# Kernel tuning notes

Hardware: AMD Instinct MI355X
Metric: run time of the kernel (lower is better)

Reference implementation:

```python
import jax, jax.numpy as jnp
import numpy as np

BN_EPS = 1e-5
LRELU_SLOPE = 0.2
EPS = 1e-8
K = 3


def setup_inputs() -> dict:
    key = jax.random.key(0)
    ks = jax.random.split(key, 8)
    B, Cd, Cs, M, S, N = 8, 256, 512, 4096, 1024, 4096
    return {
        "dense_data": jax.random.normal(ks[0], (B, Cd, M), dtype=jnp.float32),
        "dense_idx": jax.random.randint(ks[1], (B, M), 0, N),
        "sparse_data": jax.random.normal(ks[2], (B, Cs, S), dtype=jnp.float32),
        "sparse_idx": jax.random.randint(ks[3], (B, S), 0, N),
        "pcd": jax.random.normal(ks[4], (B, 3, N), dtype=jnp.float32),
        "conv_w": jax.random.normal(ks[5], (Cd, 3 * Cd), dtype=jnp.float32) * (1.0 / np.sqrt(3 * Cd)),
        "bn_gamma": jnp.ones((Cd,), dtype=jnp.float32),
        "bn_beta": jnp.zeros((Cd,), dtype=jnp.float32),
    }


def _knn_interpolate(dense_xyz, sparse_xyz, sparse_feats, k):
    # dense_xyz: [B,3,M], sparse_xyz: [B,3,S], sparse_feats: [B,Cs,S]
    d2 = (
        jnp.sum(dense_xyz**2, axis=1)[:, :, None]
        + jnp.sum(sparse_xyz**2, axis=1)[:, None, :]
        - 2.0 * jnp.einsum("bdm,bds->bms", dense_xyz, sparse_xyz)
    )  # [B,M,S] squared distances
    neg_d, idx = jax.lax.top_k(-d2, k)  # [B,M,K]
    d_nb = -neg_d
    w = 1.0 / (d_nb + EPS)
    w = w / jnp.sum(w, axis=-1, keepdims=True)  # [B,M,K]
    # gather neighbor features: [B,Cs,M,K]
    nb = jnp.take_along_axis(sparse_feats[:, :, None, :], idx[:, None, :, :], axis=3)
    return jnp.sum(nb * w[:, None, :, :], axis=-1)  # [B,Cs,M]


def reference(dense_data, dense_idx, sparse_data, sparse_idx, pcd, conv_w, bn_gamma, bn_beta):
    # gather xyz coords of dense / sparse points: [B,3,M], [B,3,S]
    dense_xyz = jnp.take_along_axis(pcd, dense_idx[:, None, :], axis=2)
    sparse_xyz = jnp.take_along_axis(pcd, sparse_idx[:, None, :], axis=2)
    interp = _knn_interpolate(dense_xyz, sparse_xyz, sparse_data, K)  # [B,Cs,M]
    x = jnp.concatenate([dense_data, interp], axis=1)  # [B,3*Cd,M]
    # 1x1 conv (no bias)
    y = jnp.einsum("oc,bcm->bom", conv_w, x)
    # BatchNorm1d (training mode: batch statistics over B and M, biased var)
    mu = jnp.mean(y, axis=(0, 2), keepdims=True)
    var = jnp.mean((y - mu) ** 2, axis=(0, 2), keepdims=True)
    y = (y - mu) * jax.lax.rsqrt(var + BN_EPS)
    y = y * bn_gamma[None, :, None] + bn_beta[None, :, None]
    # LeakyReLU(0.2)
    y = jnp.where(y >= 0, y, LRELU_SLOPE * y)
    return (y, dense_idx)
```

## Files before the change

kernel.cpp:

```cpp
#include <hip/hip_runtime.h>
#include <float.h>

#define DEVI __device__ __forceinline__

namespace {

constexpr int NB   = 8;
constexpr int CD   = 256;
constexpr int CS   = 512;
constexpr int MM   = 4096;
constexpr int SS   = 1024;
constexpr int NN   = 4096;
constexpr int KTOT = 768;
constexpr int OC   = 256;
constexpr float KEPS  = 1e-8f;
constexpr float BNEPS = 1e-5f;
constexpr float SLOPE = 0.2f;

constexpr size_t OFF_Z    = 0;
constexpr size_t SZ_Z     = (size_t)NB * SS * OC * 4;
constexpr size_t OFF_IDX3 = OFF_Z + SZ_Z;
constexpr size_t SZ_IDX3  = (size_t)NB * MM * 3 * 4;
constexpr size_t OFF_W3   = OFF_IDX3 + SZ_IDX3;
constexpr size_t OFF_WBF  = OFF_W3 + SZ_IDX3;
constexpr size_t SZ_WBF   = (size_t)OC * KTOT * 2;
constexpr size_t OFF_PS   = OFF_WBF + SZ_WBF;
constexpr size_t SZ_PS    = (size_t)512 * OC * 4;
constexpr size_t OFF_PS2  = OFF_PS + SZ_PS;
constexpr size_t OFF_A    = OFF_PS2 + SZ_PS;
constexpr size_t OFF_B    = OFF_A + 1024;

typedef __attribute__((ext_vector_type(8))) short s16x8;
typedef __attribute__((ext_vector_type(4))) float f32x4;

DEVI short f2bf(float f) {
  union { float f; unsigned u; } c; c.f = f;
  unsigned r = c.u + 0x7fffu + ((c.u >> 16) & 1u);
  return (short)(r >> 16);
}

__global__ __launch_bounds__(256) void k_knn(
    const int* __restrict__ didx, const int* __restrict__ sidx,
    const float* __restrict__ pcd,
    int* __restrict__ idx3, float* __restrict__ w3,
    float* __restrict__ outIdxF,
    const float* __restrict__ convw, short* __restrict__ wbf) {
  __shared__ float4 sxyz[SS];
  __shared__ float  pd[4][64][3];
  __shared__ int    pi[4][64][3];

  int blk = blockIdx.x;
  int b   = blk >> 6;
  int m0  = (blk & 63) << 6;
  int tid = threadIdx.x;
  const float* pb = pcd + (size_t)b * 3 * NN;

  for (int i = tid; i < 384; i += 256) {
    int g = blk * 384 + i;
    wbf[g] = f2bf(convw[g]);
  }

  for (int s = tid; s < SS; s += 256) {
    int si = sidx[b * SS + s];
    sxyz[s] = make_float4(pb[si], pb[NN + si], pb[2 * NN + si], 0.f);
  }

  int p     = tid & 63;
  int chunk = tid >> 6;
  int m     = m0 + p;
  int di    = didx[b * MM + m];
  float px = pb[di], py = pb[NN + di], pz = pb[2 * NN + di];

  if (chunk == 0) outIdxF[b * MM + m] = (float)di;

  __syncthreads();

  float d0 = FLT_MAX, d1 = FLT_MAX, d2 = FLT_MAX;
  int   i0 = 0, i1 = 0, i2 = 0;
  int s0c = chunk << 8;
#pragma unroll 4
  for (int t = 0; t < 256; ++t) {
    int s = s0c + t;
    float4 c = sxyz[s];
    float dx = c.x - px, dy = c.y - py, dz = c.z - pz;
    float d  = dx * dx + dy * dy + dz * dz;
    bool lt0 = d < d0, lt1 = d < d1, lt2 = d < d2;
    d2 = lt1 ? d1 : (lt2 ? d : d2);  i2 = lt1 ? i1 : (lt2 ? s : i2);
    d1 = lt0 ? d0 : (lt1 ? d : d1);  i1 = lt0 ? i0 : (lt1 ? s : i1);
    d0 = lt0 ? d  : d0;              i0 = lt0 ? s : i0;
  }
  pd[chunk][p][0] = d0; pd[chunk][p][1] = d1; pd[chunk][p][2] = d2;
  pi[chunk][p][0] = i0; pi[chunk][p][1] = i1; pi[chunk][p][2] = i2;
  __syncthreads();

  if (tid < 64) {
    float e0 = FLT_MAX, e1 = FLT_MAX, e2 = FLT_MAX;
    int   j0 = 0, j1 = 0, j2 = 0;
#pragma unroll
    for (int c = 0; c < 4; ++c)
#pragma unroll
      for (int r = 0; r < 3; ++r) {
        float d = pd[c][p][r]; int s = pi[c][p][r];
        bool lt0 = d < e0, lt1 = d < e1, lt2 = d < e2;
        e2 = lt1 ? e1 : (lt2 ? d : e2);  j2 = lt1 ? j1 : (lt2 ? s : j2);
        e1 = lt0 ? e0 : (lt1 ? d : e1);  j1 = lt0 ? j0 : (lt1 ? s : j1);
        e0 = lt0 ? d  : e0;              j0 = lt0 ? s : j0;
      }
    float w0 = 1.f / (e0 + KEPS), w1 = 1.f / (e1 + KEPS), w2 = 1.f / (e2 + KEPS);
    float inv = 1.f / (w0 + w1 + w2);
    int base = (b * MM + m) * 3;
    idx3[base] = j0; idx3[base + 1] = j1; idx3[base + 2] = j2;
    w3[base] = w0 * inv; w3[base + 1] = w1 * inv; w3[base + 2] = w2 * inv;
  }
}

__global__ __launch_bounds__(256) void k_gemmZ(
    const float* __restrict__ sp, const short* __restrict__ wbf,
    float* __restrict__ Z) {
  __shared__ __align__(16) short Wl[256 * 72];
  __shared__ __align__(16) short Sl[32 * 72];

  int blk = blockIdx.x;
  int st = blk & 31, b = blk >> 5;
  int s0 = st * 32;
  int tid = threadIdx.x, wv = tid >> 6, lane = tid & 63;
  int lo = lane & 15, quad = lane >> 4;

  f32x4 acc[4][2] = {};
  for (int k0 = 0; k0 < CS; k0 += 64) {
    __syncthreads();
#pragma unroll
    for (int r = 0; r < 8; ++r) {
      int lin = r * 256 + tid, row = lin >> 3, c8 = lin & 7;
      uint4 v = *(const uint4*)((const unsigned short*)wbf + (size_t)row * KTOT + CD + k0 + c8 * 8);
      *(uint4*)(&Wl[row * 72 + c8 * 8]) = v;
    }
#pragma unroll
    for (int r = 0; r < 2; ++r) {
      int lin = r * 256 + tid, cc = lin >> 3, s4 = lin & 7;
      float4 v = *(const float4*)(sp + (size_t)(b * CS + k0 + cc) * SS + s0 + s4 * 4);
      Sl[(s4 * 4 + 0) * 72 + cc] = f2bf(v.x);
      Sl[(s4 * 4 + 1) * 72 + cc] = f2bf(v.y);
      Sl[(s4 * 4 + 2) * 72 + cc] = f2bf(v.z);
      Sl[(s4 * 4 + 3) * 72 + cc] = f2bf(v.w);
    }
    __syncthreads();
    s16x8 af[2][4], bfr[2][2];
#pragma unroll
    for (int h = 0; h < 2; ++h) {
#pragma unroll
      for (int i = 0; i < 4; ++i)
        af[h][i] = *(const s16x8*)(&Wl[(wv * 64 + i * 16 + lo) * 72 + h * 32 + quad * 8]);
#pragma unroll
      for (int j = 0; j < 2; ++j)
        bfr[h][j] = *(const s16x8*)(&Sl[(j * 16 + lo) * 72 + h * 32 + quad * 8]);
    }
#pragma unroll
    for (int h = 0; h < 2; ++h)
#pragma unroll
      for (int i = 0; i < 4; ++i)
#pragma unroll
        for (int j = 0; j < 2; ++j)
          acc[i][j] = __builtin_amdgcn_mfma_f32_16x16x32_bf16(af[h][i], bfr[h][j], acc[i][j], 0, 0, 0);
  }
#pragma unroll
  for (int i = 0; i < 4; ++i)
#pragma unroll
    for (int j = 0; j < 2; ++j) {
      int s = j * 16 + lo, o = wv * 64 + i * 16 + quad * 4;
      *(f32x4*)(Z + (size_t)(b * SS + s0 + s) * OC + o) = acc[i][j];
    }
}

__global__ __launch_bounds__(256) void k_gemmDC(
    const float* __restrict__ dense, const float* __restrict__ Z,
    const int* __restrict__ idx3, const float* __restrict__ w3,
    const short* __restrict__ wbf, float* __restrict__ y,
    float* __restrict__ ps, float* __restrict__ ps2) {
  __shared__ __align__(16) short Wl[256 * 72];
  __shared__ __align__(16) short Xl[64 * 72];
  __shared__ int   mi3[192];
  __shared__ float mw3[192];

  int blk = blockIdx.x;
  int mt = blk & 63, b = blk >> 6, m0 = mt << 6;
  int tid = threadIdx.x, wv = tid >> 6, lane = tid & 63;
  int lo = lane & 15, quad = lane >> 4;

  {
    int base = (b * MM + m0) * 3;
    for (int i = tid; i < 192; i += 256) { mi3[i] = idx3[base + i]; mw3[i] = w3[base + i]; }
  }

  f32x4 acc[4][4] = {};
  for (int k0 = 0; k0 < CD; k0 += 64) {
    __syncthreads();
#pragma unroll
    for (int r = 0; r < 8; ++r) {
      int lin = r * 256 + tid, row = lin >> 3, c8 = lin & 7;
      uint4 v = *(const uint4*)((const unsigned short*)wbf + (size_t)row * KTOT + k0 + c8 * 8);
      *(uint4*)(&Wl[row * 72 + c8 * 8]) = v;
    }
    {
      int kk4 = tid >> 4, m4 = tid & 15;
      float4 v0 = *(const float4*)(dense + (size_t)(b * CD + k0 + kk4 * 4 + 0) * MM + m0 + m4 * 4);
      float4 v1 = *(const float4*)(dense + (size_t)(b * CD + k0 + kk4 * 4 + 1) * MM + m0 + m4 * 4);
      float4 v2 = *(const float4*)(dense + (size_t)(b * CD + k0 + kk4 * 4 + 2) * MM + m0 + m4 * 4);
      float4 v3 = *(const float4*)(dense + (size_t)(b * CD + k0 + kk4 * 4 + 3) * MM + m0 + m4 * 4);
      ushort4 w;
      w.x = (unsigned short)f2bf(v0.x); w.y = (unsigned short)f2bf(v1.x);
      w.z = (unsigned short)f2bf(v2.x); w.w = (unsigned short)f2bf(v3.x);
      *(ushort4*)(&Xl[(m4 * 4 + 0) * 72 + kk4 * 4]) = w;
      w.x = (unsigned short)f2bf(v0.y); w.y = (unsigned short)f2bf(v1.y);
      w.z = (unsigned short)f2bf(v2.y); w.w = (unsigned short)f2bf(v3.y);
      *(ushort4*)(&Xl[(m4 * 4 + 1) * 72 + kk4 * 4]) = w;
      w.x = (unsigned short)f2bf(v0.z); w.y = (unsigned short)f2bf(v1.z);
      w.z = (unsigned short)f2bf(v2.z); w.w = (unsigned short)f2bf(v3.z);
      *(ushort4*)(&Xl[(m4 * 4 + 2) * 72 + kk4 * 4]) = w;
      w.x = (unsigned short)f2bf(v0.w); w.y = (unsigned short)f2bf(v1.w);
      w.z = (unsigned short)f2bf(v2.w); w.w = (unsigned short)f2bf(v3.w);
      *(ushort4*)(&Xl[(m4 * 4 + 3) * 72 + kk4 * 4]) = w;
    }
    __syncthreads();
    s16x8 af[2][4], bfr[2][4];
#pragma unroll
    for (int h = 0; h < 2; ++h) {
#pragma unroll
      for (int i = 0; i < 4; ++i)
        af[h][i] = *(const s16x8*)(&Wl[(wv * 64 + i * 16 + lo) * 72 + h * 32 + quad * 8]);
#pragma unroll
      for (int j = 0; j < 4; ++j)
        bfr[h][j] = *(const s16x8*)(&Xl[(j * 16 + lo) * 72 + h * 32 + quad * 8]);
    }
#pragma unroll
    for (int h = 0; h < 2; ++h)
#pragma unroll
      for (int i = 0; i < 4; ++i)
#pragma unroll
        for (int j = 0; j < 4; ++j)
          acc[i][j] = __builtin_amdgcn_mfma_f32_16x16x32_bf16(af[h][i], bfr[h][j], acc[i][j], 0, 0, 0);
  }

  float* P = (float*)Wl;
  const float* Zb = Z + (size_t)b * SS * OC;
  float ss[4][4] = {}, s2s[4][4] = {};
  __syncthreads();

#pragma unroll
  for (int h = 0; h < 2; ++h) {
#pragma unroll 4
    for (int ml = 0; ml < 32; ++ml) {
      int mg = (h * 32 + ml) * 3;
      float p = mw3[mg + 0] * Zb[(size_t)mi3[mg + 0] * OC + tid]
              + mw3[mg + 1] * Zb[(size_t)mi3[mg + 1] * OC + tid]
              + mw3[mg + 2] * Zb[(size_t)mi3[mg + 2] * OC + tid];
      P[ml * 260 + tid] = p;
    }
    __syncthreads();
#pragma unroll
    for (int i = 0; i < 4; ++i)
#pragma unroll
      for (int jj = 0; jj < 2; ++jj) {
        int j = h * 2 + jj, ml = jj * 16 + lo;
        int o = wv * 64 + i * 16 + quad * 4;
        f32x4 p = *(const f32x4*)(&P[ml * 260 + o]);
        f32x4 v = acc[i][j] + p;
        float* dst = y + (size_t)(b * OC + o) * MM + m0 + j * 16 + lo;
#pragma unroll
        for (int r = 0; r < 4; ++r) {
          float vv = v[r];
          dst[(size_t)r * MM] = vv;
          ss[i][r] += vv; s2s[i][r] += vv * vv;
        }
      }
    __syncthreads();
  }

#pragma unroll
  for (int i = 0; i < 4; ++i)
#pragma unroll
    for (int r = 0; r < 4; ++r) {
      float a = ss[i][r], q = s2s[i][r];
      for (int off = 1; off < 16; off <<= 1) { a += __shfl_xor(a, off); q += __shfl_xor(q, off); }
      ss[i][r] = a; s2s[i][r] = q;
    }
  if (lo == 0) {
#pragma unroll
    for (int i = 0; i < 4; ++i)
#pragma unroll
      for (int r = 0; r < 4; ++r) {
        int o = wv * 64 + i * 16 + quad * 4 + r;
        ps[(size_t)blk * OC + o]  = ss[i][r];
        ps2[(size_t)blk * OC + o] = s2s[i][r];
      }
  }
}

__global__ void k_finalize(const float* __restrict__ ps, const float* __restrict__ ps2,
                           const float* __restrict__ gamma, const float* __restrict__ beta,
                           float* __restrict__ sA, float* __restrict__ sB) {
  int o = threadIdx.x;
  float s = 0.f, s2 = 0.f;
#pragma unroll 8
  for (int k = 0; k < 512; ++k) { s += ps[k * OC + o]; s2 += ps2[k * OC + o]; }
  float mn = s / (float)(NB * MM);
  float vr = s2 / (float)(NB * MM) - mn * mn;
  float a  = rsqrtf(vr + BNEPS) * gamma[o];
  sA[o] = a;
  sB[o] = beta[o] - mn * a;
}

__global__ void k_norm(float* __restrict__ y, const float* __restrict__ sA,
                       const float* __restrict__ sB) {
  int i = blockIdx.x * 256 + threadIdx.x;
  int o = (i >> 10) & 255;
  float a = sA[o], be = sB[o];
  float4 v = ((const float4*)y)[i];
  float t;
  t = v.x * a + be; v.x = t >= 0.f ? t : SLOPE * t;
  t = v.y * a + be; v.y = t >= 0.f ? t : SLOPE * t;
  t = v.z * a + be; v.z = t >= 0.f ? t : SLOPE * t;
  t = v.w * a + be; v.w = t >= 0.f ? t : SLOPE * t;
  ((float4*)y)[i] = v;
}

}

extern "C" void kernel_launch(void* const* d_in, const int* in_sizes, int n_in,
                              void* d_out, int out_size, void* d_ws, size_t ws_size,
                              hipStream_t stream) {
  const float* dense = (const float*)d_in[0];
  const int*   didx  = (const int*)d_in[1];
  const float* sp    = (const float*)d_in[2];
  const int*   sidx  = (const int*)d_in[3];
  const float* pcd   = (const float*)d_in[4];
  const float* convw = (const float*)d_in[5];
  const float* gamma = (const float*)d_in[6];
  const float* beta  = (const float*)d_in[7];

  float* y = (float*)d_out;
  float* outIdxF = y + (size_t)NB * OC * MM;

  char* ws = (char*)d_ws;
  float* Z    = (float*)(ws + OFF_Z);
  int*   idx3 = (int*)(ws + OFF_IDX3);
  float* w3   = (float*)(ws + OFF_W3);
  short* wbf  = (short*)(ws + OFF_WBF);
  float* ps   = (float*)(ws + OFF_PS);
  float* ps2  = (float*)(ws + OFF_PS2);
  float* sA   = (float*)(ws + OFF_A);
  float* sB   = (float*)(ws + OFF_B);

  k_knn     <<<NB * (MM / 64), 256, 0, stream>>>(didx, sidx, pcd, idx3, w3, outIdxF, convw, wbf);
  k_gemmZ   <<<NB * (SS / 32), 256, 0, stream>>>(sp, wbf, Z);
  k_gemmDC  <<<NB * (MM / 64), 256, 0, stream>>>(dense, Z, idx3, w3, wbf, y, ps, ps2);
  k_finalize<<<1, 256, 0, stream>>>(ps, ps2, gamma, beta, sA, sB);
  k_norm    <<<(NB * OC * MM / 4) / 256, 256, 0, stream>>>(y, sA, sB);
}
```

Before: 193.5 us.

## Merge kNN and sparse GEMM into one launch; convert weights inline; direct Z gather

```diff
diff --git a/kernel.cpp b/kernel.cpp
--- a/kernel.cpp
+++ b/kernel.cpp
@@ -22,9 +22,7 @@
 constexpr size_t OFF_IDX3 = OFF_Z + SZ_Z;
 constexpr size_t SZ_IDX3  = (size_t)NB * MM * 3 * 4;
 constexpr size_t OFF_W3   = OFF_IDX3 + SZ_IDX3;
-constexpr size_t OFF_WBF  = OFF_W3 + SZ_IDX3;
-constexpr size_t SZ_WBF   = (size_t)OC * KTOT * 2;
-constexpr size_t OFF_PS   = OFF_WBF + SZ_WBF;
+constexpr size_t OFF_PS   = OFF_W3 + SZ_IDX3;
 constexpr size_t SZ_PS    = (size_t)512 * OC * 4;
 constexpr size_t OFF_PS2  = OFF_PS + SZ_PS;
 constexpr size_t OFF_A    = OFF_PS2 + SZ_PS;
@@ -39,143 +37,146 @@
   return (short)(r >> 16);
 }
 
-__global__ __launch_bounds__(256) void k_knn(
+__global__ __launch_bounds__(256) void k_pre(
     const int* __restrict__ didx, const int* __restrict__ sidx,
-    const float* __restrict__ pcd,
+    const float* __restrict__ pcd, const float* __restrict__ sp,
+    const float* __restrict__ convw,
     int* __restrict__ idx3, float* __restrict__ w3,
-    float* __restrict__ outIdxF,
-    const float* __restrict__ convw, short* __restrict__ wbf) {
-  __shared__ float4 sxyz[SS];
-  __shared__ float  pd[4][64][3];
-  __shared__ int    pi[4][64][3];
-
-  int blk = blockIdx.x;
-  int b   = blk >> 6;
-  int m0  = (blk & 63) << 6;
+    float* __restrict__ outIdxF, float* __restrict__ Z) {
+  __shared__ __align__(16) char smem[41472];
+
   int tid = threadIdx.x;
-  const float* pb = pcd + (size_t)b * 3 * NN;
-
-  for (int i = tid; i < 384; i += 256) {
-    int g = blk * 384 + i;
-    wbf[g] = f2bf(convw[g]);
-  }
-
-  for (int s = tid; s < SS; s += 256) {
-    int si = sidx[b * SS + s];
-    sxyz[s] = make_float4(pb[si], pb[NN + si], pb[2 * NN + si], 0.f);
-  }
-
-  int p     = tid & 63;
-  int chunk = tid >> 6;
-  int m     = m0 + p;
-  int di    = didx[b * MM + m];
-  float px = pb[di], py = pb[NN + di], pz = pb[2 * NN + di];
-
-  if (chunk == 0) outIdxF[b * MM + m] = (float)di;
-
-  __syncthreads();
-
-  float d0 = FLT_MAX, d1 = FLT_MAX, d2 = FLT_MAX;
-  int   i0 = 0, i1 = 0, i2 = 0;
-  int s0c = chunk << 8;
+
+  if (blockIdx.x < 512) {
+    float4* sxyz = (float4*)smem;
+    float*  pd   = (float*)(smem + 16384);
+    int*    pi   = (int*)(smem + 16384 + 3072);
+
+    int blk = blockIdx.x;
+    int b   = blk >> 6;
+    int m0  = (blk & 63) << 6;
+    const float* pb = pcd + (size_t)b * 3 * NN;
+
+    for (int s = tid; s < SS; s += 256) {
+      int si = sidx[b * SS + s];
+      sxyz[s] = make_float4(pb[si], pb[NN + si], pb[2 * NN + si], 0.f);
+    }
+
+    int p     = tid & 63;
+    int chunk = tid >> 6;
+    int m     = m0 + p;
+    int di    = didx[b * MM + m];
+    float px = pb[di], py = pb[NN + di], pz = pb[2 * NN + di];
+
+    if (chunk == 0) outIdxF[b * MM + m] = (float)di;
+
+    __syncthreads();
+
+    float d0 = FLT_MAX, d1 = FLT_MAX, d2 = FLT_MAX;
+    int   i0 = 0, i1 = 0, i2 = 0;
+    int s0c = chunk << 8;
 #pragma unroll 4
-  for (int t = 0; t < 256; ++t) {
-    int s = s0c + t;
-    float4 c = sxyz[s];
-    float dx = c.x - px, dy = c.y - py, dz = c.z - pz;
-    float d  = dx * dx + dy * dy + dz * dz;
-    bool lt0 = d < d0, lt1 = d < d1, lt2 = d < d2;
-    d2 = lt1 ? d1 : (lt2 ? d : d2);  i2 = lt1 ? i1 : (lt2 ? s : i2);
-    d1 = lt0 ? d0 : (lt1 ? d : d1);  i1 = lt0 ? i0 : (lt1 ? s : i1);
-    d0 = lt0 ? d  : d0;              i0 = lt0 ? s : i0;
-  }
-  pd[chunk][p][0] = d0; pd[chunk][p][1] = d1; pd[chunk][p][2] = d2;
-  pi[chunk][p][0] = i0; pi[chunk][p][1] = i1; pi[chunk][p][2] = i2;
-  __syncthreads();
-
-  if (tid < 64) {
-    float e0 = FLT_MAX, e1 = FLT_MAX, e2 = FLT_MAX;
-    int   j0 = 0, j1 = 0, j2 = 0;
-#pragma unroll
-    for (int c = 0; c < 4; ++c)
-#pragma unroll
-      for (int r = 0; r < 3; ++r) {
-        float d = pd[c][p][r]; int s = pi[c][p][r];
-        bool lt0 = d < e0, lt1 = d < e1, lt2 = d < e2;
-        e2 = lt1 ? e1 : (lt2 ? d : e2);  j2 = lt1 ? j1 : (lt2 ? s : j2);
-        e1 = lt0 ? e0 : (lt1 ? d : e1);  j1 = lt0 ? j0 : (lt1 ? s : j1);
-        e0 = lt0 ? d  : e0;              j0 = lt0 ? s : j0;
-      }
-    float w0 = 1.f / (e0 + KEPS), w1 = 1.f / (e1 + KEPS), w2 = 1.f / (e2 + KEPS);
-    float inv = 1.f / (w0 + w1 + w2);
-    int base = (b * MM + m) * 3;
-    idx3[base] = j0; idx3[base + 1] = j1; idx3[base + 2] = j2;
-    w3[base] = w0 * inv; w3[base + 1] = w1 * inv; w3[base + 2] = w2 * inv;
-  }
-}
-
-__global__ __launch_bounds__(256) void k_gemmZ(
-    const float* __restrict__ sp, const short* __restrict__ wbf,
-    float* __restrict__ Z) {
-  __shared__ __align__(16) short Wl[256 * 72];
-  __shared__ __align__(16) short Sl[32 * 72];
-
-  int blk = blockIdx.x;
-  int st = blk & 31, b = blk >> 5;
-  int s0 = st * 32;
-  int tid = threadIdx.x, wv = tid >> 6, lane = tid & 63;
-  int lo = lane & 15, quad = lane >> 4;
-
-  f32x4 acc[4][2] = {};
-  for (int k0 = 0; k0 < CS; k0 += 64) {
+    for (int t = 0; t < 256; ++t) {
+      int s = s0c + t;
+      float4 c = sxyz[s];
+      float dx = c.x - px, dy = c.y - py, dz = c.z - pz;
+      float d  = dx * dx + dy * dy + dz * dz;
+      bool lt0 = d < d0, lt1 = d < d1, lt2 = d < d2;
+      d2 = lt1 ? d1 : (lt2 ? d : d2);  i2 = lt1 ? i1 : (lt2 ? s : i2);
+      d1 = lt0 ? d0 : (lt1 ? d : d1);  i1 = lt0 ? i0 : (lt1 ? s : i1);
+      d0 = lt0 ? d  : d0;              i0 = lt0 ? s : i0;
+    }
+    pd[(chunk * 64 + p) * 3 + 0] = d0; pd[(chunk * 64 + p) * 3 + 1] = d1; pd[(chunk * 64 + p) * 3 + 2] = d2;
+    pi[(chunk * 64 + p) * 3 + 0] = i0; pi[(chunk * 64 + p) * 3 + 1] = i1; pi[(chunk * 64 + p) * 3 + 2] = i2;
     __syncthreads();
-#pragma unroll
-    for (int r = 0; r < 8; ++r) {
-      int lin = r * 256 + tid, row = lin >> 3, c8 = lin & 7;
-      uint4 v = *(const uint4*)((const unsigned short*)wbf + (size_t)row * KTOT + CD + k0 + c8 * 8);
-      *(uint4*)(&Wl[row * 72 + c8 * 8]) = v;
-    }
-#pragma unroll
-    for (int r = 0; r < 2; ++r) {
-      int lin = r * 256 + tid, cc = lin >> 3, s4 = lin & 7;
-      float4 v = *(const float4*)(sp + (size_t)(b * CS + k0 + cc) * SS + s0 + s4 * 4);
-      Sl[(s4 * 4 + 0) * 72 + cc] = f2bf(v.x);
-      Sl[(s4 * 4 + 1) * 72 + cc] = f2bf(v.y);
-      Sl[(s4 * 4 + 2) * 72 + cc] = f2bf(v.z);
-      Sl[(s4 * 4 + 3) * 72 + cc] = f2bf(v.w);
-    }
-    __syncthreads();
-    s16x8 af[2][4], bfr[2][2];
-#pragma unroll
-    for (int h = 0; h < 2; ++h) {
-#pragma unroll
-      for (int i = 0; i < 4; ++i)
-        af[h][i] = *(const s16x8*)(&Wl[(wv * 64 + i * 16 + lo) * 72 + h * 32 + quad * 8]);
-#pragma unroll
-      for (int j = 0; j < 2; ++j)
-        bfr[h][j] = *(const s16x8*)(&Sl[(j * 16 + lo) * 72 + h * 32 + quad * 8]);
-    }
-#pragma unroll
-    for (int h = 0; h < 2; ++h)
-#pragma unroll
-      for (int i = 0; i < 4; ++i)
+
+    if (tid < 64) {
+      float e0 = FLT_MAX, e1 = FLT_MAX, e2 = FLT_MAX;
+      int   j0 = 0, j1 = 0, j2 = 0;
+#pragma unroll
+      for (int c = 0; c < 4; ++c)
+#pragma unroll
+        for (int r = 0; r < 3; ++r) {
+          float d = pd[(c * 64 + p) * 3 + r]; int s = pi[(c * 64 + p) * 3 + r];
+          bool lt0 = d < e0, lt1 = d < e1, lt2 = d < e2;
+          e2 = lt1 ? e1 : (lt2 ? d : e2);  j2 = lt1 ? j1 : (lt2 ? s : j2);
+          e1 = lt0 ? e0 : (lt1 ? d : e1);  j1 = lt0 ? j0 : (lt1 ? s : j1);
+          e0 = lt0 ? d  : e0;              j0 = lt0 ? s : j0;
+        }
+      float w0 = 1.f / (e0 + KEPS), w1 = 1.f / (e1 + KEPS), w2 = 1.f / (e2 + KEPS);
+      float inv = 1.f / (w0 + w1 + w2);
+      int base = (b * MM + m) * 3;
+      idx3[base] = j0; idx3[base + 1] = j1; idx3[base + 2] = j2;
+      w3[base] = w0 * inv; w3[base + 1] = w1 * inv; w3[base + 2] = w2 * inv;
+    }
+  } else {
+    short* Wl = (short*)smem;
+    short* Sl = (short*)(smem + 256 * 72 * 2);
+
+    int blk = blockIdx.x - 512;
+    int st = blk & 31, b = blk >> 5;
+    int s0 = st * 32;
+    int wv = tid >> 6, lane = tid & 63;
+    int lo = lane & 15, quad = lane >> 4;
+
+    f32x4 acc[4][2] = {};
+    for (int k0 = 0; k0 < CS; k0 += 64) {
+      __syncthreads();
+#pragma unroll
+      for (int r = 0; r < 8; ++r) {
+        int lin = r * 256 + tid, row = lin >> 3, c8 = lin & 7;
+        const float* src = convw + (size_t)row * KTOT + CD + k0 + c8 * 8;
+        float4 va = *(const float4*)src, vb = *(const float4*)(src + 4);
+        ushort4 plo, phi;
+        plo.x = (unsigned short)f2bf(va.x); plo.y = (unsigned short)f2bf(va.y);
+        plo.z = (unsigned short)f2bf(va.z); plo.w = (unsigned short)f2bf(va.w);
+        phi.x = (unsigned short)f2bf(vb.x); phi.y = (unsigned short)f2bf(vb.y);
+        phi.z = (unsigned short)f2bf(vb.z); phi.w = (unsigned short)f2bf(vb.w);
+        *(ushort4*)(&Wl[row * 72 + c8 * 8])     = plo;
+        *(ushort4*)(&Wl[row * 72 + c8 * 8 + 4]) = phi;
+      }
+#pragma unroll
+      for (int r = 0; r < 2; ++r) {
+        int lin = r * 256 + tid, cc = lin >> 3, s4 = lin & 7;
+        float4 v = *(const float4*)(sp + (size_t)(b * CS + k0 + cc) * SS + s0 + s4 * 4);
+        Sl[(s4 * 4 + 0) * 72 + cc] = f2bf(v.x);
+        Sl[(s4 * 4 + 1) * 72 + cc] = f2bf(v.y);
+        Sl[(s4 * 4 + 2) * 72 + cc] = f2bf(v.z);
+        Sl[(s4 * 4 + 3) * 72 + cc] = f2bf(v.w);
+      }
+      __syncthreads();
+      s16x8 af[2][4], bfr[2][2];
+#pragma unroll
+      for (int h = 0; h < 2; ++h) {
+#pragma unroll
+        for (int i = 0; i < 4; ++i)
+          af[h][i] = *(const s16x8*)(&Wl[(wv * 64 + i * 16 + lo) * 72 + h * 32 + quad * 8]);
 #pragma unroll
         for (int j = 0; j < 2; ++j)
-          acc[i][j] = __builtin_amdgcn_mfma_f32_16x16x32_bf16(af[h][i], bfr[h][j], acc[i][j], 0, 0, 0);
-  }
-#pragma unroll
-  for (int i = 0; i < 4; ++i)
-#pragma unroll
-    for (int j = 0; j < 2; ++j) {
-      int s = j * 16 + lo, o = wv * 64 + i * 16 + quad * 4;
-      *(f32x4*)(Z + (size_t)(b * SS + s0 + s) * OC + o) = acc[i][j];
-    }
+          bfr[h][j] = *(const s16x8*)(&Sl[(j * 16 + lo) * 72 + h * 32 + quad * 8]);
+      }
+#pragma unroll
+      for (int h = 0; h < 2; ++h)
+#pragma unroll
+        for (int i = 0; i < 4; ++i)
+#pragma unroll
+          for (int j = 0; j < 2; ++j)
+            acc[i][j] = __builtin_amdgcn_mfma_f32_16x16x32_bf16(af[h][i], bfr[h][j], acc[i][j], 0, 0, 0);
+    }
+#pragma unroll
+    for (int i = 0; i < 4; ++i)
+#pragma unroll
+      for (int j = 0; j < 2; ++j) {
+        int s = j * 16 + lo, o = wv * 64 + i * 16 + quad * 4;
+        *(f32x4*)(Z + (size_t)(b * SS + s0 + s) * OC + o) = acc[i][j];
+      }
+  }
 }
 
 __global__ __launch_bounds__(256) void k_gemmDC(
     const float* __restrict__ dense, const float* __restrict__ Z,
     const int* __restrict__ idx3, const float* __restrict__ w3,
-    const short* __restrict__ wbf, float* __restrict__ y,
+    const float* __restrict__ convw, float* __restrict__ y,
     float* __restrict__ ps, float* __restrict__ ps2) {
   __shared__ __align__(16) short Wl[256 * 72];
   __shared__ __align__(16) short Xl[64 * 72];
@@ -198,8 +199,15 @@
 #pragma unroll
     for (int r = 0; r < 8; ++r) {
       int lin = r * 256 + tid, row = lin >> 3, c8 = lin & 7;
-      uint4 v = *(const uint4*)((const unsigned short*)wbf + (size_t)row * KTOT + k0 + c8 * 8);
-      *(uint4*)(&Wl[row * 72 + c8 * 8]) = v;
+      const float* src = convw + (size_t)row * KTOT + k0 + c8 * 8;
+      float4 va = *(const float4*)src, vb = *(const float4*)(src + 4);
+      ushort4 plo, phi;
+      plo.x = (unsigned short)f2bf(va.x); plo.y = (unsigned short)f2bf(va.y);
+      plo.z = (unsigned short)f2bf(va.z); plo.w = (unsigned short)f2bf(va.w);
+      phi.x = (unsigned short)f2bf(vb.x); phi.y = (unsigned short)f2bf(vb.y);
+      phi.z = (unsigned short)f2bf(vb.z); phi.w = (unsigned short)f2bf(vb.w);
+      *(ushort4*)(&Wl[row * 72 + c8 * 8])     = plo;
+      *(ushort4*)(&Wl[row * 72 + c8 * 8 + 4]) = phi;
     }
     {
       int kk4 = tid >> 4, m4 = tid & 15;
@@ -241,39 +249,31 @@
           acc[i][j] = __builtin_amdgcn_mfma_f32_16x16x32_bf16(af[h][i], bfr[h][j], acc[i][j], 0, 0, 0);
   }
 
-  float* P = (float*)Wl;
   const float* Zb = Z + (size_t)b * SS * OC;
   float ss[4][4] = {}, s2s[4][4] = {};
-  __syncthreads();
-
-#pragma unroll
-  for (int h = 0; h < 2; ++h) {
-#pragma unroll 4
-    for (int ml = 0; ml < 32; ++ml) {
-      int mg = (h * 32 + ml) * 3;
-      float p = mw3[mg + 0] * Zb[(size_t)mi3[mg + 0] * OC + tid]
-              + mw3[mg + 1] * Zb[(size_t)mi3[mg + 1] * OC + tid]
-              + mw3[mg + 2] * Zb[(size_t)mi3[mg + 2] * OC + tid];
-      P[ml * 260 + tid] = p;
-    }
-    __syncthreads();
-#pragma unroll
-    for (int i = 0; i < 4; ++i)
-#pragma unroll
-      for (int jj = 0; jj < 2; ++jj) {
-        int j = h * 2 + jj, ml = jj * 16 + lo;
-        int o = wv * 64 + i * 16 + quad * 4;
-        f32x4 p = *(const f32x4*)(&P[ml * 260 + o]);
-        f32x4 v = acc[i][j] + p;
-        float* dst = y + (size_t)(b * OC + o) * MM + m0 + j * 16 + lo;
-#pragma unroll
-        for (int r = 0; r < 4; ++r) {
-          float vv = v[r];
-          dst[(size_t)r * MM] = vv;
-          ss[i][r] += vv; s2s[i][r] += vv * vv;
-        }
-      }
-    __syncthreads();
+#pragma unroll
+  for (int j = 0; j < 4; ++j) {
+    int ml = j * 16 + lo;
+    int r0 = mi3[ml * 3 + 0], r1 = mi3[ml * 3 + 1], r2 = mi3[ml * 3 + 2];
+    float w0 = mw3[ml * 3 + 0], w1 = mw3[ml * 3 + 1], w2 = mw3[ml * 3 + 2];
+    const float* z0 = Zb + (size_t)r0 * OC;
+    const float* z1 = Zb + (size_t)r1 * OC;
+    const float* z2 = Zb + (size_t)r2 * OC;
+#pragma unroll
+    for (int i = 0; i < 4; ++i) {
+      int o = wv * 64 + i * 16 + quad * 4;
+      f32x4 p = w0 * *(const f32x4*)(z0 + o)
+              + w1 * *(const f32x4*)(z1 + o)
+              + w2 * *(const f32x4*)(z2 + o);
+      f32x4 v = acc[i][j] + p;
+      float* dst = y + (size_t)(b * OC + o) * MM + m0 + ml;
+#pragma unroll
+      for (int r = 0; r < 4; ++r) {
+        float vv = v[r];
+        dst[(size_t)r * MM] = vv;
+        ss[i][r] += vv; s2s[i][r] += vv * vv;
+      }
+    }
   }
 
 #pragma unroll
@@ -345,15 +345,13 @@
   float* Z    = (float*)(ws + OFF_Z);
   int*   idx3 = (int*)(ws + OFF_IDX3);
   float* w3   = (float*)(ws + OFF_W3);
-  short* wbf  = (short*)(ws + OFF_WBF);
   float* ps   = (float*)(ws + OFF_PS);
   float* ps2  = (float*)(ws + OFF_PS2);
   float* sA   = (float*)(ws + OFF_A);
   float* sB   = (float*)(ws + OFF_B);
 
-  k_knn     <<<NB * (MM / 64), 256, 0, stream>>>(didx, sidx, pcd, idx3, w3, outIdxF, convw, wbf);
-  k_gemmZ   <<<NB * (SS / 32), 256, 0, stream>>>(sp, wbf, Z);
-  k_gemmDC  <<<NB * (MM / 64), 256, 0, stream>>>(dense, Z, idx3, w3, wbf, y, ps, ps2);
+  k_pre     <<<768, 256, 0, stream>>>(didx, sidx, pcd, sp, convw, idx3, w3, outIdxF, Z);
+  k_gemmDC  <<<NB * (MM / 64), 256, 0, stream>>>(dense, Z, idx3, w3, convw, y, ps, ps2);
   k_finalize<<<1, 256, 0, stream>>>(ps, ps2, gamma, beta, sA, sB);
   k_norm    <<<(NB * OC * MM / 4) / 256, 256, 0, stream>>>(y, sA, sB);
 }
```

New measurement: 207.9 us. 7.5% more time.

## Pack KNN distance and index into sortable keys; parallelize BN finalize

Applied to the files above, without the earlier changes.

```diff
diff --git a/kernel.cpp b/kernel.cpp
--- a/kernel.cpp
+++ b/kernel.cpp
@@ -39,15 +39,17 @@
   return (short)(r >> 16);
 }
 
+DEVI unsigned umin_(unsigned a, unsigned b) { return a < b ? a : b; }
+DEVI unsigned umax_(unsigned a, unsigned b) { return a > b ? a : b; }
+
 __global__ __launch_bounds__(256) void k_knn(
     const int* __restrict__ didx, const int* __restrict__ sidx,
     const float* __restrict__ pcd,
     int* __restrict__ idx3, float* __restrict__ w3,
     float* __restrict__ outIdxF,
     const float* __restrict__ convw, short* __restrict__ wbf) {
-  __shared__ float4 sxyz[SS];
-  __shared__ float  pd[4][64][3];
-  __shared__ int    pi[4][64][3];
+  __shared__ float4   sxyz[SS];
+  __shared__ unsigned pk[4][64][3];
 
   int blk = blockIdx.x;
   int b   = blk >> 6;
@@ -62,7 +64,8 @@
 
   for (int s = tid; s < SS; s += 256) {
     int si = sidx[b * SS + s];
-    sxyz[s] = make_float4(pb[si], pb[NN + si], pb[2 * NN + si], 0.f);
+    float x = pb[si], yy = pb[NN + si], z = pb[2 * NN + si];
+    sxyz[s] = make_float4(x, yy, z, x * x + yy * yy + z * z);
   }
 
   int p     = tid & 63;
@@ -70,42 +73,46 @@
   int m     = m0 + p;
   int di    = didx[b * MM + m];
   float px = pb[di], py = pb[NN + di], pz = pb[2 * NN + di];
+  float pp = px * px + py * py + pz * pz;
+  float nx = -2.f * px, ny = -2.f * py, nz = -2.f * pz;
 
   if (chunk == 0) outIdxF[b * MM + m] = (float)di;
 
   __syncthreads();
 
-  float d0 = FLT_MAX, d1 = FLT_MAX, d2 = FLT_MAX;
-  int   i0 = 0, i1 = 0, i2 = 0;
+  unsigned k0 = 0xFFFFFFFFu, k1 = 0xFFFFFFFFu, k2 = 0xFFFFFFFFu;
   int s0c = chunk << 8;
 #pragma unroll 4
   for (int t = 0; t < 256; ++t) {
     int s = s0c + t;
     float4 c = sxyz[s];
-    float dx = c.x - px, dy = c.y - py, dz = c.z - pz;
-    float d  = dx * dx + dy * dy + dz * dz;
-    bool lt0 = d < d0, lt1 = d < d1, lt2 = d < d2;
-    d2 = lt1 ? d1 : (lt2 ? d : d2);  i2 = lt1 ? i1 : (lt2 ? s : i2);
-    d1 = lt0 ? d0 : (lt1 ? d : d1);  i1 = lt0 ? i0 : (lt1 ? s : i1);
-    d0 = lt0 ? d  : d0;              i0 = lt0 ? s : i0;
-  }
-  pd[chunk][p][0] = d0; pd[chunk][p][1] = d1; pd[chunk][p][2] = d2;
-  pi[chunk][p][0] = i0; pi[chunk][p][1] = i1; pi[chunk][p][2] = i2;
+    float d = fmaf(nx, c.x, c.w + pp);
+    d = fmaf(ny, c.y, d);
+    d = fmaf(nz, c.z, d);
+    d = fmaxf(d, 0.f);
+    unsigned key = (__float_as_uint(d) & 0xFFFFFC00u) | (unsigned)s;
+    unsigned e0 = umax_(key, k0); k0 = umin_(key, k0);
+    unsigned e1 = umax_(e0, k1);  k1 = umin_(e0, k1);
+    k2 = umin_(e1, k2);
+  }
+  pk[chunk][p][0] = k0; pk[chunk][p][1] = k1; pk[chunk][p][2] = k2;
   __syncthreads();
 
   if (tid < 64) {
-    float e0 = FLT_MAX, e1 = FLT_MAX, e2 = FLT_MAX;
-    int   j0 = 0, j1 = 0, j2 = 0;
+    unsigned g0 = 0xFFFFFFFFu, g1 = 0xFFFFFFFFu, g2 = 0xFFFFFFFFu;
 #pragma unroll
     for (int c = 0; c < 4; ++c)
 #pragma unroll
       for (int r = 0; r < 3; ++r) {
-        float d = pd[c][p][r]; int s = pi[c][p][r];
-        bool lt0 = d < e0, lt1 = d < e1, lt2 = d < e2;
-        e2 = lt1 ? e1 : (lt2 ? d : e2);  j2 = lt1 ? j1 : (lt2 ? s : j2);
-        e1 = lt0 ? e0 : (lt1 ? d : e1);  j1 = lt0 ? j0 : (lt1 ? s : j1);
-        e0 = lt0 ? d  : e0;              j0 = lt0 ? s : j0;
+        unsigned key = pk[c][p][r];
+        unsigned e0 = umax_(key, g0); g0 = umin_(key, g0);
+        unsigned e1 = umax_(e0, g1);  g1 = umin_(e0, g1);
+        g2 = umin_(e1, g2);
       }
+    int j0 = g0 & 1023, j1 = g1 & 1023, j2 = g2 & 1023;
+    float e0 = __uint_as_float(g0 & 0xFFFFFC00u);
+    float e1 = __uint_as_float(g1 & 0xFFFFFC00u);
+    float e2 = __uint_as_float(g2 & 0xFFFFFC00u);
     float w0 = 1.f / (e0 + KEPS), w1 = 1.f / (e1 + KEPS), w2 = 1.f / (e2 + KEPS);
     float inv = 1.f / (w0 + w1 + w2);
     int base = (b * MM + m) * 3;
@@ -299,15 +306,32 @@
 __global__ void k_finalize(const float* __restrict__ ps, const float* __restrict__ ps2,
                            const float* __restrict__ gamma, const float* __restrict__ beta,
                            float* __restrict__ sA, float* __restrict__ sB) {
-  int o = threadIdx.x;
+  __shared__ float red[512];
+  int blk = blockIdx.x;
+  int tid = threadIdx.x;
+  int ch = tid & 31, sl = tid >> 5;
+  int o = blk * 32 + ch;
   float s = 0.f, s2 = 0.f;
-#pragma unroll 8
-  for (int k = 0; k < 512; ++k) { s += ps[k * OC + o]; s2 += ps2[k * OC + o]; }
-  float mn = s / (float)(NB * MM);
-  float vr = s2 / (float)(NB * MM) - mn * mn;
-  float a  = rsqrtf(vr + BNEPS) * gamma[o];
-  sA[o] = a;
-  sB[o] = beta[o] - mn * a;
+#pragma unroll 4
+  for (int j = 0; j < 64; ++j) {
+    int k = sl * 64 + j;
+    s  += ps[(size_t)k * OC + o];
+    s2 += ps2[(size_t)k * OC + o];
+  }
+  red[sl * 32 + ch] = s;
+  red[256 + sl * 32 + ch] = s2;
+  __syncthreads();
+  if (tid < 32) {
+    float S = 0.f, S2 = 0.f;
+#pragma unroll
+    for (int t = 0; t < 8; ++t) { S += red[t * 32 + tid]; S2 += red[256 + t * 32 + tid]; }
+    int oo = blk * 32 + tid;
+    float mn = S / (float)(NB * MM);
+    float vr = S2 / (float)(NB * MM) - mn * mn;
+    float a  = rsqrtf(vr + BNEPS) * gamma[oo];
+    sA[oo] = a;
+    sB[oo] = beta[oo] - mn * a;
+  }
 }
 
 __global__ void k_norm(float* __restrict__ y, const float* __restrict__ sA,
@@ -354,6 +378,6 @@
   k_knn     <<<NB * (MM / 64), 256, 0, stream>>>(didx, sidx, pcd, idx3, w3, outIdxF, convw, wbf);
   k_gemmZ   <<<NB * (SS / 32), 256, 0, stream>>>(sp, wbf, Z);
   k_gemmDC  <<<NB * (MM / 64), 256, 0, stream>>>(dense, Z, idx3, w3, wbf, y, ps, ps2);
-  k_finalize<<<1, 256, 0, stream>>>(ps, ps2, gamma, beta, sA, sB);
+  k_finalize<<<8, 256, 0, stream>>>(ps, ps2, gamma, beta, sA, sB);
   k_norm    <<<(NB * OC * MM / 4) / 256, 256, 0, stream>>>(y, sA, sB);
 }
```

Result: faster. 164.9 us (-14.8%).
